# Kernel tuning notes

Hardware: AMD Instinct MI355X
Metric: run time of the kernel (lower is better)

Reference implementation:

```python
import jax, jax.numpy as jnp
import numpy as np

MODEL_DIM = 1024
BATCH, SEQ = 4, 2048


def setup_inputs() -> dict:
    key = jax.random.key(0)
    kx, kq, kk, kv = jax.random.split(key, 4)
    s = 1.0 / np.sqrt(MODEL_DIM)
    return {
        "x": jax.random.normal(kx, (BATCH, SEQ, MODEL_DIM), dtype=jnp.float32),
        "Wq": jax.random.normal(kq, (MODEL_DIM, MODEL_DIM), dtype=jnp.float32) * s,
        "Wk": jax.random.normal(kk, (MODEL_DIM, MODEL_DIM), dtype=jnp.float32) * s,
        "Wv": jax.random.normal(kv, (MODEL_DIM, MODEL_DIM), dtype=jnp.float32) * s,
    }


def reference(x, Wq, Wk, Wv):
    # nn.Linear(d, d, bias=False): y = x @ W.T ; W stored [out, in]
    q = jnp.einsum("bsd,ed->bse", x, Wq)
    k = jnp.einsum("bsd,ed->bse", x, Wk)
    v = jnp.einsum("bsd,ed->bse", x, Wv)
    scores = jnp.einsum("bqd,bkd->bqk", q, k) / jnp.sqrt(jnp.float32(MODEL_DIM))
    attn = jax.nn.softmax(scores, axis=-1)
    return jnp.einsum("bqk,bkd->bqd", attn, v)
```

## Files before the change

### kernel.cpp

```cpp
#include <hip/hip_runtime.h>
#include <hip/hip_bf16.h>


typedef short bf16x8_t __attribute__((ext_vector_type(8)));
typedef float f32x4_t __attribute__((ext_vector_type(4)));
typedef unsigned short u16x8_t __attribute__((ext_vector_type(8)));

static __device__ __forceinline__ unsigned short f2bf(float f) {
  __hip_bfloat16 h = __float2bfloat16(f);
  return *reinterpret_cast<unsigned short*>(&h);
}

#define GLOAD_LDS16(gp, lp)                                            \
  __builtin_amdgcn_global_load_lds(                                    \
      (const __attribute__((address_space(1))) void*)(gp),             \
      (__attribute__((address_space(3))) void*)(lp), 16, 0, 0)

__global__ __launch_bounds__(256) void cast_f32_bf16(
    const float* __restrict__ in, unsigned short* __restrict__ out, int n8) {
  int i = blockIdx.x * 256 + threadIdx.x;
  if (i >= n8) return;
  float4 a = ((const float4*)in)[i * 2];
  float4 b = ((const float4*)in)[i * 2 + 1];
  u16x8_t o;
  o[0] = f2bf(a.x); o[1] = f2bf(a.y); o[2] = f2bf(a.z); o[3] = f2bf(a.w);
  o[4] = f2bf(b.x); o[5] = f2bf(b.y); o[6] = f2bf(b.z); o[7] = f2bf(b.w);
  ((u16x8_t*)out)[i] = o;
}

__global__ __launch_bounds__(256) void cast_w3(
    const float* __restrict__ Wq, const float* __restrict__ Wk,
    const float* __restrict__ Wv, unsigned short* __restrict__ Wqk,
    unsigned short* __restrict__ Wvb) {
  int i = blockIdx.x * 256 + threadIdx.x;
  int seg = i >> 17;
  int local = i & 131071;
  const float* src = (seg == 0) ? Wq : ((seg == 1) ? Wk : Wv);
  unsigned short* dst =
      (seg == 0) ? Wqk : ((seg == 1) ? (Wqk + 1048576) : Wvb);
  float4 a = ((const float4*)src)[local * 2];
  float4 b = ((const float4*)src)[local * 2 + 1];
  u16x8_t o;
  o[0] = f2bf(a.x); o[1] = f2bf(a.y); o[2] = f2bf(a.z); o[3] = f2bf(a.w);
  o[4] = f2bf(b.x); o[5] = f2bf(b.y); o[6] = f2bf(b.z); o[7] = f2bf(b.w);
  ((u16x8_t*)dst)[local] = o;
}

__global__ __launch_bounds__(256) void zero_f32(float* __restrict__ p, int n) {
  int i = blockIdx.x * 256 + threadIdx.x;
  if (i < n) p[i] = 0.0f;
}

template <int EPI>
__global__ __launch_bounds__(512, 2) void gemm256_nt(
    const unsigned short* __restrict__ A, const unsigned short* __restrict__ B,
    unsigned short* __restrict__ C, float* __restrict__ rowsum, int K,
    int lda, int ldb, int ldc, long long sA, long long sB, long long sC,
    float alpha, int rsz) {
  __shared__ unsigned short lds[2][2][256 * 64];

  const int gx = gridDim.x, gy = gridDim.y;
  const int nwg = gx * gy * gridDim.z;
  const int orig = (blockIdx.z * gy + blockIdx.y) * gx + blockIdx.x;
  const int swz = (orig & 7) * (nwg >> 3) + (orig >> 3);
  const int bx = swz % gx;
  const int tmp = swz / gx;
  const int by = tmp % gy;
  const int z = tmp / gy;

  const int tid = threadIdx.x;
  const int lane = tid & 63;
  const int w = tid >> 6;
  const int wm = w >> 2, wn = w & 3;
  const int m0 = by * 256, n0 = bx * 256;

  A += (long long)z * sA;
  B += (long long)z * sB;

  int sar[4], sac[4];
#pragma unroll
  for (int i = 0; i < 4; ++i) {
    int p = i * 512 + w * 64 + lane;
    int r = p >> 3;
    sar[i] = r;
    sac[i] = ((p & 7) ^ (r & 7)) * 8;
  }

  const int q = lane >> 4, rl = lane & 15;
  int aoff[8][2], boff[4][2];
#pragma unroll
  for (int t = 0; t < 8; ++t)
#pragma unroll
    for (int ks = 0; ks < 2; ++ks) {
      int ra = wm * 128 + t * 16 + rl;
      int ca = ks * 4 + q;
      aoff[t][ks] = ra * 64 + ((ca ^ (ra & 7)) * 8);
    }
#pragma unroll
  for (int u = 0; u < 4; ++u)
#pragma unroll
    for (int ks = 0; ks < 2; ++ks) {
      int rb = wn * 64 + u * 16 + rl;
      int ca = ks * 4 + q;
      boff[u][ks] = rb * 64 + ((ca ^ (rb & 7)) * 8);
    }

  f32x4_t acc[8][4];
#pragma unroll
  for (int i = 0; i < 8; ++i)
#pragma unroll
    for (int j = 0; j < 4; ++j) acc[i][j] = (f32x4_t){0.f, 0.f, 0.f, 0.f};

#define STAGE256(bufi, k0)                                                   \
  {                                                                          \
    _Pragma("unroll") for (int i = 0; i < 4; ++i)                            \
        GLOAD_LDS16(&A[(long long)(m0 + sar[i]) * lda + (k0) + sac[i]],      \
                    &lds[bufi][0][(i * 512 + w * 64) * 8]);                  \
    _Pragma("unroll") for (int i = 0; i < 4; ++i)                            \
        GLOAD_LDS16(&B[(long long)(n0 + sar[i]) * ldb + (k0) + sac[i]],      \
                    &lds[bufi][1][(i * 512 + w * 64) * 8]);                  \
  }

  const int NT = K >> 6;
  STAGE256(0, 0);
  STAGE256(1, 64);

  for (int t = 0; t < NT; ++t) {
    const int cur = t & 1;
    if (t < NT - 1)
      asm volatile("s_waitcnt vmcnt(8)" ::: "memory");
    else
      asm volatile("s_waitcnt vmcnt(0)" ::: "memory");
    __builtin_amdgcn_s_barrier();
    __builtin_amdgcn_sched_barrier(0);
    const unsigned short* Al = &lds[cur][0][0];
    const unsigned short* Bl = &lds[cur][1][0];
#pragma unroll
    for (int ks = 0; ks < 2; ++ks) {
      bf16x8_t af[8], bg[4];
#pragma unroll
      for (int tt = 0; tt < 8; ++tt)
        af[tt] = *(const bf16x8_t*)&Al[aoff[tt][ks]];
#pragma unroll
      for (int u = 0; u < 4; ++u) bg[u] = *(const bf16x8_t*)&Bl[boff[u][ks]];
      __builtin_amdgcn_s_setprio(1);
#pragma unroll
      for (int i = 0; i < 8; ++i)
#pragma unroll
        for (int j = 0; j < 4; ++j)
          acc[i][j] = __builtin_amdgcn_mfma_f32_16x16x32_bf16(af[i], bg[j],
                                                              acc[i][j], 0, 0, 0);
      __builtin_amdgcn_s_setprio(0);
    }
    __builtin_amdgcn_sched_barrier(0);
    __builtin_amdgcn_s_barrier();
    __builtin_amdgcn_sched_barrier(0);
    if (t + 2 < NT) STAGE256(cur, (t + 2) * 64);
  }

  if (EPI == 0) {
#pragma unroll
    for (int tt = 0; tt < 8; ++tt)
#pragma unroll
      for (int u = 0; u < 4; ++u)
#pragma unroll
        for (int j = 0; j < 4; ++j) {
          int row = m0 + wm * 128 + tt * 16 + q * 4 + j;
          int col = n0 + wn * 64 + u * 16 + rl;
          C[(long long)z * sC + (long long)row * ldc + col] =
              f2bf(acc[tt][u][j] * alpha);
        }
  } else {
#pragma unroll
    for (int tt = 0; tt < 8; ++tt)
#pragma unroll
      for (int j = 0; j < 4; ++j) {
        int row = m0 + wm * 128 + tt * 16 + q * 4 + j;
        float sum = 0.f;
#pragma unroll
        for (int u = 0; u < 4; ++u) {
          float e = __expf(acc[tt][u][j] * alpha);
          int col = n0 + wn * 64 + u * 16 + rl;
          C[(long long)z * sC + (long long)row * ldc + col] = f2bf(e);
          sum += e;
        }
#pragma unroll
        for (int mk = 1; mk <= 8; mk <<= 1) sum += __shfl_xor(sum, mk);
        if (rl == 0) atomicAdd(&rowsum[z * rsz + row], sum);
      }
  }
#undef STAGE256
}

template <int EPI, int BN>
__global__ __launch_bounds__(256) void gemm_nt(
    const unsigned short* __restrict__ A, const unsigned short* __restrict__ B,
    void* __restrict__ Cv, const float* __restrict__ rowsum, int M, int N,
    int K, int lda, int ldb, int ldc, long long sA, long long sB,
    long long sC, float alpha, int rsz) {
  constexpr int NB = BN / 32;
  __shared__ unsigned short As[128 * 64];
  __shared__ unsigned short Bs[BN * 64];

  const int gx = gridDim.x, gy = gridDim.y;
  const int nwg = gx * gy * gridDim.z;
  const int orig = (blockIdx.z * gy + blockIdx.y) * gx + blockIdx.x;
  const int swz = (orig & 7) * (nwg >> 3) + (orig >> 3);
  const int bx = swz % gx;
  const int tmp = swz / gx;
  const int by = tmp % gy;
  const int z = tmp / gy;

  const int tid = threadIdx.x;
  const int lane = tid & 63;
  const int w = tid >> 6;
  const int wm = w >> 1, wn = w & 1;
  const int m0 = by * 128;
  const int n0 = bx * BN;

  A += (long long)z * sA;
  B += (long long)z * sB;

  int sarow[4], sacol[4];
#pragma unroll
  for (int i = 0; i < 4; ++i) {
    int p = w * 256 + i * 64 + lane;
    int r = p >> 3;
    sarow[i] = r;
    sacol[i] = ((p & 7) ^ (r & 7)) * 8;
  }
  int sbrow[NB], sbcol[NB];
#pragma unroll
  for (int i = 0; i < NB; ++i) {
    int p = w * (BN * 2) + i * 64 + lane;
    int r = p >> 3;
    sbrow[i] = r;
    sbcol[i] = ((p & 7) ^ (r & 7)) * 8;
  }

  const int q = lane >> 4, rl = lane & 15;
  int aoff[4][2], boff[NB][2];
#pragma unroll
  for (int t = 0; t < 4; ++t)
#pragma unroll
    for (int ks = 0; ks < 2; ++ks) {
      int ra = wm * 64 + t * 16 + rl;
      int ca = ks * 4 + q;
      aoff[t][ks] = ra * 64 + ((ca ^ (ra & 7)) * 8);
    }
#pragma unroll
  for (int u = 0; u < NB; ++u)
#pragma unroll
    for (int ks = 0; ks < 2; ++ks) {
      int rb = wn * (BN / 2) + u * 16 + rl;
      int ca = ks * 4 + q;
      boff[u][ks] = rb * 64 + ((ca ^ (rb & 7)) * 8);
    }

  f32x4_t acc[4][NB];
#pragma unroll
  for (int i = 0; i < 4; ++i)
#pragma unroll
    for (int j = 0; j < NB; ++j) acc[i][j] = (f32x4_t){0.f, 0.f, 0.f, 0.f};

  for (int k0 = 0; k0 < K; k0 += 64) {
    __syncthreads();
#pragma unroll
    for (int i = 0; i < 4; ++i) {
      GLOAD_LDS16(&A[(long long)(m0 + sarow[i]) * lda + k0 + sacol[i]],
                  &As[(w * 4 + i) * 512]);
    }
#pragma unroll
    for (int i = 0; i < NB; ++i) {
      GLOAD_LDS16(&B[(long long)(n0 + sbrow[i]) * ldb + k0 + sbcol[i]],
                  &Bs[(w * NB + i) * 512]);
    }
    __syncthreads();

#pragma unroll
    for (int ks = 0; ks < 2; ++ks) {
      bf16x8_t af[4], bg[NB];
#pragma unroll
      for (int t = 0; t < 4; ++t) af[t] = *(const bf16x8_t*)&As[aoff[t][ks]];
#pragma unroll
      for (int u = 0; u < NB; ++u) bg[u] = *(const bf16x8_t*)&Bs[boff[u][ks]];
#pragma unroll
      for (int i = 0; i < 4; ++i)
#pragma unroll
        for (int j = 0; j < NB; ++j)
          acc[i][j] = __builtin_amdgcn_mfma_f32_16x16x32_bf16(af[i], bg[j],
                                                              acc[i][j], 0, 0, 0);
    }
  }

#pragma unroll
  for (int t = 0; t < 4; ++t)
#pragma unroll
    for (int u = 0; u < NB; ++u)
#pragma unroll
      for (int j = 0; j < 4; ++j) {
        int row = m0 + wm * 64 + t * 16 + q * 4 + j;
        int col = n0 + wn * (BN / 2) + u * 16 + rl;
        if (EPI == 0) {
          ((unsigned short*)Cv)[(long long)z * sC + (long long)row * ldc +
                                col] = f2bf(acc[t][u][j] * alpha);
        } else if (EPI == 1) {
          ((float*)Cv)[(long long)z * sC + (long long)row * ldc + col] =
              acc[t][u][j] * alpha;
        } else {
          float inv = 1.0f / rowsum[z * rsz + row];
          ((float*)Cv)[(long long)z * sC + (long long)row * ldc + col] =
              acc[t][u][j] * inv;
        }
      }
}

extern "C" void kernel_launch(void* const* d_in, const int* in_sizes, int n_in,
                              void* d_out, int out_size, void* d_ws,
                              size_t ws_size, hipStream_t stream) {
  const float* x = (const float*)d_in[0];
  const float* Wq = (const float*)d_in[1];
  const float* Wk = (const float*)d_in[2];
  const float* Wv = (const float*)d_in[3];
  float* out = (float*)d_out;

  unsigned short* xb = (unsigned short*)d_ws;
  unsigned short* Wqk = xb + 8388608;
  unsigned short* Wvb = Wqk + 2097152;
  unsigned short* Cqk = Wvb + 1048576;
  unsigned short* VTb = Cqk + 16777216;
  unsigned short* Scb = VTb + 8388608;
  float* rowsumf = (float*)(Scb + 16777216);

  const dim3 blk(256);
  const dim3 blk512(512);

  cast_f32_bf16<<<4096, blk, 0, stream>>>(x, xb, 1048576);
  cast_w3<<<1536, blk, 0, stream>>>(Wq, Wk, Wv, Wqk, Wvb);
  zero_f32<<<32, blk, 0, stream>>>(rowsumf, 8192);

  gemm256_nt<0><<<dim3(8, 32, 1), blk512, 0, stream>>>(
      xb, Wqk, Cqk, nullptr, 1024, 1024, 1024, 2048, 0, 0, 0, 1.0f, 0);

  gemm_nt<0, 128><<<dim3(64, 8, 1), blk, 0, stream>>>(
      Wvb, xb, VTb, nullptr, 1024, 8192, 1024, 1024, 1024, 8192, 0, 0, 0,
      1.0f, 0);

  gemm256_nt<1><<<dim3(8, 8, 4), blk512, 0, stream>>>(
      Cqk, Cqk + 1024, Scb, rowsumf, 1024, 2048, 2048, 2048,
      (long long)2048 * 2048, (long long)2048 * 2048, (long long)2048 * 2048,
      0.03125f, 2048);

  gemm_nt<2, 64><<<dim3(16, 16, 4), blk, 0, stream>>>(
      Scb, VTb, out, rowsumf, 2048, 1024, 2048, 2048, 8192, 1024,
      (long long)2048 * 2048, 2048, (long long)2048 * 1024, 1.0f, 2048);
}
```

Baseline: 169.7 us.

## Split 256-tile GEMM into four-phase pipelined quadrants and use it for PV

The 256-row GEMM main loop is restructured into four MFMA phases over quadrants of the tile, each with its own barrier. Global-to-LDS loads for the next k-steps are issued in halves between phases so memory traffic interleaves with matrix math. The kernel is templated on N tile width and gains a normalizing fp32 epilogue, so the final attention-times-V GEMM now runs on 256x128 tiles with 512 threads instead of the small 128x64 kernel. The extra barriers and finer-grained vmcnt waits add synchronization, and the load ordering is tricky to get right.

```diff
diff --git a/kernel.cpp b/kernel.cpp
--- a/kernel.cpp
+++ b/kernel.cpp
@@ -51,13 +51,20 @@
   if (i < n) p[i] = 0.0f;
 }
 
-template <int EPI>
-__global__ __launch_bounds__(512, 2) void gemm256_nt(
+template <int EPI, int BN>
+__global__ __launch_bounds__(512, 2) void gemm256p(
     const unsigned short* __restrict__ A, const unsigned short* __restrict__ B,
-    unsigned short* __restrict__ C, float* __restrict__ rowsum, int K,
-    int lda, int ldb, int ldc, long long sA, long long sB, long long sC,
-    float alpha, int rsz) {
-  __shared__ unsigned short lds[2][2][256 * 64];
+    void* __restrict__ Cv, float* __restrict__ rowsum, int K, int lda,
+    int ldb, int ldc, long long sA, long long sB, long long sC, float alpha,
+    int rsz) {
+  constexpr int NBG = BN / 64;
+  constexpr int NH = NBG / 2;
+  constexpr int BL = BN / 128;
+  constexpr int BNW = BN / 4;
+  constexpr int ASZ = 256 * 64;
+  constexpr int BSZ = BN * 64;
+
+  __shared__ unsigned short lds[2][ASZ + BSZ];
 
   const int gx = gridDim.x, gy = gridDim.y;
   const int nwg = gx * gy * gridDim.z;
@@ -72,105 +79,160 @@
   const int lane = tid & 63;
   const int w = tid >> 6;
   const int wm = w >> 2, wn = w & 3;
-  const int m0 = by * 256, n0 = bx * 256;
+  const int m0 = by * 256, n0 = bx * BN;
 
   A += (long long)z * sA;
   B += (long long)z * sB;
 
-  int sar[4], sac[4];
-#pragma unroll
-  for (int i = 0; i < 4; ++i) {
-    int p = i * 512 + w * 64 + lane;
-    int r = p >> 3;
-    sar[i] = r;
-    sac[i] = ((p & 7) ^ (r & 7)) * 8;
-  }
+  int sta_row[2][2], sta_col[2][2], sta_lds[2][2];
+#pragma unroll
+  for (int mh = 0; mh < 2; ++mh)
+#pragma unroll
+    for (int i = 0; i < 2; ++i) {
+      int j = w * 2 + i;
+      int l0 = (j >> 3) * 1024 + mh * 512 + (j & 7) * 64;
+      int lf = l0 + lane;
+      int R = lf >> 3;
+      sta_row[mh][i] = R;
+      sta_col[mh][i] = ((lf & 7) ^ (R & 7)) * 8;
+      sta_lds[mh][i] = l0 * 8;
+    }
+  int stb_row[2][BL], stb_col[2][BL], stb_lds[2][BL];
+#pragma unroll
+  for (int nh = 0; nh < 2; ++nh)
+#pragma unroll
+    for (int i = 0; i < BL; ++i) {
+      int l0;
+      if (BL == 2) {
+        int j = w * 2 + i;
+        l0 = (j >> 2) * 512 + nh * 256 + (j & 3) * 64;
+      } else {
+        int j = w;
+        l0 = (j >> 1) * 256 + nh * 128 + (j & 1) * 64;
+      }
+      int lf = l0 + lane;
+      int R = lf >> 3;
+      stb_row[nh][i] = R;
+      stb_col[nh][i] = ((lf & 7) ^ (R & 7)) * 8;
+      stb_lds[nh][i] = ASZ + l0 * 8;
+    }
 
   const int q = lane >> 4, rl = lane & 15;
-  int aoff[8][2], boff[4][2];
-#pragma unroll
-  for (int t = 0; t < 8; ++t)
+  int aoff[8][2], boff[NBG][2];
+#pragma unroll
+  for (int tt = 0; tt < 8; ++tt)
 #pragma unroll
     for (int ks = 0; ks < 2; ++ks) {
-      int ra = wm * 128 + t * 16 + rl;
-      int ca = ks * 4 + q;
-      aoff[t][ks] = ra * 64 + ((ca ^ (ra & 7)) * 8);
-    }
-#pragma unroll
-  for (int u = 0; u < 4; ++u)
+      int ra = wm * 128 + tt * 16 + rl;
+      aoff[tt][ks] = ra * 64 + (((ks * 4 + q) ^ (ra & 7)) * 8);
+    }
+#pragma unroll
+  for (int u = 0; u < NBG; ++u)
 #pragma unroll
     for (int ks = 0; ks < 2; ++ks) {
-      int rb = wn * 64 + u * 16 + rl;
-      int ca = ks * 4 + q;
-      boff[u][ks] = rb * 64 + ((ca ^ (rb & 7)) * 8);
-    }
-
-  f32x4_t acc[8][4];
+      int rb = wn * BNW + u * 16 + rl;
+      boff[u][ks] = ASZ + rb * 64 + (((ks * 4 + q) ^ (rb & 7)) * 8);
+    }
+
+  f32x4_t acc[8][NBG];
 #pragma unroll
   for (int i = 0; i < 8; ++i)
 #pragma unroll
-    for (int j = 0; j < 4; ++j) acc[i][j] = (f32x4_t){0.f, 0.f, 0.f, 0.f};
-
-#define STAGE256(bufi, k0)                                                   \
-  {                                                                          \
-    _Pragma("unroll") for (int i = 0; i < 4; ++i)                            \
-        GLOAD_LDS16(&A[(long long)(m0 + sar[i]) * lda + (k0) + sac[i]],      \
-                    &lds[bufi][0][(i * 512 + w * 64) * 8]);                  \
-    _Pragma("unroll") for (int i = 0; i < 4; ++i)                            \
-        GLOAD_LDS16(&B[(long long)(n0 + sar[i]) * ldb + (k0) + sac[i]],      \
-                    &lds[bufi][1][(i * 512 + w * 64) * 8]);                  \
-  }
+    for (int j = 0; j < NBG; ++j) acc[i][j] = (f32x4_t){0.f, 0.f, 0.f, 0.f};
+
+#define SA(BUFI, MH, K0)                                                    \
+  {                                                                         \
+    _Pragma("unroll") for (int i_ = 0; i_ < 2; ++i_)                        \
+        GLOAD_LDS16(&A[(long long)(m0 + sta_row[MH][i_]) * lda + (K0) +     \
+                       sta_col[MH][i_]],                                    \
+                    &lds[BUFI][sta_lds[MH][i_]]);                           \
+  }
+#define SB(BUFI, NH_, K0)                                                   \
+  {                                                                         \
+    _Pragma("unroll") for (int i_ = 0; i_ < BL; ++i_)                       \
+        GLOAD_LDS16(&B[(long long)(n0 + stb_row[NH_][i_]) * ldb + (K0) +    \
+                       stb_col[NH_][i_]],                                   \
+                    &lds[BUFI][stb_lds[NH_][i_]]);                          \
+  }
+#define LDAF(MH)                                                            \
+  _Pragma("unroll") for (int i_ = 0; i_ < 4; ++i_)                          \
+  _Pragma("unroll") for (int ks_ = 0; ks_ < 2; ++ks_)                       \
+      af[i_][ks_] = *(const bf16x8_t*)&L[aoff[(MH)*4 + i_][ks_]];
+#define LDBG(NH_)                                                           \
+  _Pragma("unroll") for (int j_ = 0; j_ < NH; ++j_)                         \
+  _Pragma("unroll") for (int ks_ = 0; ks_ < 2; ++ks_)                       \
+      bg[j_][ks_] = *(const bf16x8_t*)&L[boff[(NH_)*NH + j_][ks_]];
+#define PH_MFMA(MH, NH_)                                                    \
+  __builtin_amdgcn_s_barrier();                                             \
+  asm volatile("s_waitcnt lgkmcnt(0)" ::: "memory");                        \
+  __builtin_amdgcn_sched_barrier(0);                                        \
+  __builtin_amdgcn_s_setprio(1);                                            \
+  _Pragma("unroll") for (int ks_ = 0; ks_ < 2; ++ks_)                       \
+  _Pragma("unroll") for (int i_ = 0; i_ < 4; ++i_)                          \
+  _Pragma("unroll") for (int j_ = 0; j_ < NH; ++j_)                         \
+      acc[(MH)*4 + i_][(NH_)*NH + j_] =                                     \
+          __builtin_amdgcn_mfma_f32_16x16x32_bf16(                          \
+              af[i_][ks_], bg[j_][ks_], acc[(MH)*4 + i_][(NH_)*NH + j_],    \
+              0, 0, 0);                                                     \
+  __builtin_amdgcn_s_setprio(0);                                            \
+  __builtin_amdgcn_sched_barrier(0);                                        \
+  __builtin_amdgcn_s_barrier();                                             \
+  __builtin_amdgcn_sched_barrier(0);
 
   const int NT = K >> 6;
-  STAGE256(0, 0);
-  STAGE256(1, 64);
+
+  SA(0, 0, 0); SA(0, 1, 0); SB(0, 0, 0); SB(0, 1, 0);
+  SA(1, 0, 64); SB(1, 1, 64);
+  if (BL == 2)
+    asm volatile("s_waitcnt vmcnt(4)" ::: "memory");
+  else
+    asm volatile("s_waitcnt vmcnt(3)" ::: "memory");
+  __builtin_amdgcn_s_barrier();
+  __builtin_amdgcn_sched_barrier(0);
+
+  bf16x8_t af[4][2], bg[NH][2];
 
   for (int t = 0; t < NT; ++t) {
-    const int cur = t & 1;
-    if (t < NT - 1)
-      asm volatile("s_waitcnt vmcnt(8)" ::: "memory");
-    else
+    const int bu = t & 1, nx = bu ^ 1;
+    const unsigned short* L = lds[bu];
+    const bool p1 = (t + 1 < NT), p2 = (t + 2 < NT);
+    LDAF(0);
+    LDBG(0);
+    if (p1) SA(nx, 1, (t + 1) * 64);
+    PH_MFMA(0, 0);
+    LDBG(1);
+    if (p1) SB(nx, 0, (t + 1) * 64);
+    PH_MFMA(0, 1);
+    LDAF(1);
+    if (p2) SA(bu, 0, (t + 2) * 64);
+    PH_MFMA(1, 1);
+    LDBG(0);
+    if (p2) {
+      SB(bu, 1, (t + 2) * 64);
+      if (BL == 2)
+        asm volatile("s_waitcnt vmcnt(4)" ::: "memory");
+      else
+        asm volatile("s_waitcnt vmcnt(3)" ::: "memory");
+    } else {
       asm volatile("s_waitcnt vmcnt(0)" ::: "memory");
-    __builtin_amdgcn_s_barrier();
-    __builtin_amdgcn_sched_barrier(0);
-    const unsigned short* Al = &lds[cur][0][0];
-    const unsigned short* Bl = &lds[cur][1][0];
-#pragma unroll
-    for (int ks = 0; ks < 2; ++ks) {
-      bf16x8_t af[8], bg[4];
-#pragma unroll
-      for (int tt = 0; tt < 8; ++tt)
-        af[tt] = *(const bf16x8_t*)&Al[aoff[tt][ks]];
-#pragma unroll
-      for (int u = 0; u < 4; ++u) bg[u] = *(const bf16x8_t*)&Bl[boff[u][ks]];
-      __builtin_amdgcn_s_setprio(1);
-#pragma unroll
-      for (int i = 0; i < 8; ++i)
-#pragma unroll
-        for (int j = 0; j < 4; ++j)
-          acc[i][j] = __builtin_amdgcn_mfma_f32_16x16x32_bf16(af[i], bg[j],
-                                                              acc[i][j], 0, 0, 0);
-      __builtin_amdgcn_s_setprio(0);
-    }
-    __builtin_amdgcn_sched_barrier(0);
-    __builtin_amdgcn_s_barrier();
-    __builtin_amdgcn_sched_barrier(0);
-    if (t + 2 < NT) STAGE256(cur, (t + 2) * 64);
+    }
+    PH_MFMA(1, 0);
   }
 
   if (EPI == 0) {
+    unsigned short* C = (unsigned short*)Cv + (long long)z * sC;
 #pragma unroll
     for (int tt = 0; tt < 8; ++tt)
 #pragma unroll
-      for (int u = 0; u < 4; ++u)
+      for (int u = 0; u < NBG; ++u)
 #pragma unroll
         for (int j = 0; j < 4; ++j) {
           int row = m0 + wm * 128 + tt * 16 + q * 4 + j;
-          int col = n0 + wn * 64 + u * 16 + rl;
-          C[(long long)z * sC + (long long)row * ldc + col] =
-              f2bf(acc[tt][u][j] * alpha);
+          int col = n0 + wn * BNW + u * 16 + rl;
+          C[(long long)row * ldc + col] = f2bf(acc[tt][u][j] * alpha);
         }
-  } else {
+  } else if (EPI == 1) {
+    unsigned short* C = (unsigned short*)Cv + (long long)z * sC;
 #pragma unroll
     for (int tt = 0; tt < 8; ++tt)
 #pragma unroll
@@ -178,68 +240,69 @@
         int row = m0 + wm * 128 + tt * 16 + q * 4 + j;
         float sum = 0.f;
 #pragma unroll
-        for (int u = 0; u < 4; ++u) {
+        for (int u = 0; u < NBG; ++u) {
           float e = __expf(acc[tt][u][j] * alpha);
-          int col = n0 + wn * 64 + u * 16 + rl;
-          C[(long long)z * sC + (long long)row * ldc + col] = f2bf(e);
+          int col = n0 + wn * BNW + u * 16 + rl;
+          C[(long long)row * ldc + col] = f2bf(e);
           sum += e;
         }
 #pragma unroll
         for (int mk = 1; mk <= 8; mk <<= 1) sum += __shfl_xor(sum, mk);
         if (rl == 0) atomicAdd(&rowsum[z * rsz + row], sum);
       }
-  }
-#undef STAGE256
-}
-
-template <int EPI, int BN>
-__global__ __launch_bounds__(256) void gemm_nt(
+  } else {
+    float* C = (float*)Cv + (long long)z * sC;
+#pragma unroll
+    for (int tt = 0; tt < 8; ++tt)
+#pragma unroll
+      for (int j = 0; j < 4; ++j) {
+        int row = m0 + wm * 128 + tt * 16 + q * 4 + j;
+        float inv = 1.0f / rowsum[z * rsz + row];
+#pragma unroll
+        for (int u = 0; u < NBG; ++u) {
+          int col = n0 + wn * BNW + u * 16 + rl;
+          C[(long long)row * ldc + col] = acc[tt][u][j] * inv;
+        }
+      }
+  }
+#undef SA
+#undef SB
+#undef LDAF
+#undef LDBG
+#undef PH_MFMA
+}
+
+__global__ __launch_bounds__(256) void gemm_nt128(
     const unsigned short* __restrict__ A, const unsigned short* __restrict__ B,
-    void* __restrict__ Cv, const float* __restrict__ rowsum, int M, int N,
-    int K, int lda, int ldb, int ldc, long long sA, long long sB,
-    long long sC, float alpha, int rsz) {
-  constexpr int NB = BN / 32;
+    unsigned short* __restrict__ C, int K, int lda, int ldb, int ldc) {
   __shared__ unsigned short As[128 * 64];
-  __shared__ unsigned short Bs[BN * 64];
+  __shared__ unsigned short Bs[128 * 64];
 
   const int gx = gridDim.x, gy = gridDim.y;
-  const int nwg = gx * gy * gridDim.z;
-  const int orig = (blockIdx.z * gy + blockIdx.y) * gx + blockIdx.x;
+  const int nwg = gx * gy;
+  const int orig = blockIdx.y * gx + blockIdx.x;
   const int swz = (orig & 7) * (nwg >> 3) + (orig >> 3);
   const int bx = swz % gx;
-  const int tmp = swz / gx;
-  const int by = tmp % gy;
-  const int z = tmp / gy;
+  const int by = swz / gx;
 
   const int tid = threadIdx.x;
   const int lane = tid & 63;
   const int w = tid >> 6;
   const int wm = w >> 1, wn = w & 1;
   const int m0 = by * 128;
-  const int n0 = bx * BN;
-
-  A += (long long)z * sA;
-  B += (long long)z * sB;
-
-  int sarow[4], sacol[4];
+  const int n0 = bx * 128;
+
+  int srow[4], scol[4];
 #pragma unroll
   for (int i = 0; i < 4; ++i) {
     int p = w * 256 + i * 64 + lane;
     int r = p >> 3;
-    sarow[i] = r;
-    sacol[i] = ((p & 7) ^ (r & 7)) * 8;
-  }
-  int sbrow[NB], sbcol[NB];
-#pragma unroll
-  for (int i = 0; i < NB; ++i) {
-    int p = w * (BN * 2) + i * 64 + lane;
-    int r = p >> 3;
-    sbrow[i] = r;
-    sbcol[i] = ((p & 7) ^ (r & 7)) * 8;
+    srow[i] = r;
+    scol[i] = ((p & 7) ^ (r & 7)) * 8;
   }
 
   const int q = lane >> 4, rl = lane & 15;
-  int aoff[4][2], boff[NB][2];
+  int aoff[4][2], boff[4][2];
 #pragma unroll
   for (int t = 0; t < 4; ++t)
 #pragma unroll
@@ -247,71 +310,52 @@
       int ra = wm * 64 + t * 16 + rl;
       int ca = ks * 4 + q;
       aoff[t][ks] = ra * 64 + ((ca ^ (ra & 7)) * 8);
-    }
-#pragma unroll
-  for (int u = 0; u < NB; ++u)
-#pragma unroll
-    for (int ks = 0; ks < 2; ++ks) {
-      int rb = wn * (BN / 2) + u * 16 + rl;
-      int ca = ks * 4 + q;
-      boff[u][ks] = rb * 64 + ((ca ^ (rb & 7)) * 8);
-    }
-
-  f32x4_t acc[4][NB];
+      int rb = wn * 64 + t * 16 + rl;
+      boff[t][ks] = rb * 64 + ((ca ^ (rb & 7)) * 8);
+    }
+
+  f32x4_t acc[4][4];
 #pragma unroll
   for (int i = 0; i < 4; ++i)
 #pragma unroll
-    for (int j = 0; j < NB; ++j) acc[i][j] = (f32x4_t){0.f, 0.f, 0.f, 0.f};
+    for (int j = 0; j < 4; ++j) acc[i][j] = (f32x4_t){0.f, 0.f, 0.f, 0.f};
 
   for (int k0 = 0; k0 < K; k0 += 64) {
     __syncthreads();
 #pragma unroll
     for (int i = 0; i < 4; ++i) {
-      GLOAD_LDS16(&A[(long long)(m0 + sarow[i]) * lda + k0 + sacol[i]],
+      GLOAD_LDS16(&A[(long long)(m0 + srow[i]) * lda + k0 + scol[i]],
                   &As[(w * 4 + i) * 512]);
-    }
-#pragma unroll
-    for (int i = 0; i < NB; ++i) {
-      GLOAD_LDS16(&B[(long long)(n0 + sbrow[i]) * ldb + k0 + sbcol[i]],
-                  &Bs[(w * NB + i) * 512]);
+      GLOAD_LDS16(&B[(long long)(n0 + srow[i]) * ldb + k0 + scol[i]],
+                  &Bs[(w * 4 + i) * 512]);
     }
     __syncthreads();
 
 #pragma unroll
     for (int ks = 0; ks < 2; ++ks) {
-      bf16x8_t af[4], bg[NB];
+      bf16x8_t af[4], bgv[4];
 #pragma unroll
       for (int t = 0; t < 4; ++t) af[t] = *(const bf16x8_t*)&As[aoff[t][ks]];
 #pragma unroll
-      for (int u = 0; u < NB; ++u) bg[u] = *(const bf16x8_t*)&Bs[boff[u][ks]];
+      for (int u = 0; u < 4; ++u) bgv[u] = *(const bf16x8_t*)&Bs[boff[u][ks]];
 #pragma unroll
       for (int i = 0; i < 4; ++i)
 #pragma unroll
-        for (int j = 0; j < NB; ++j)
-          acc[i][j] = __builtin_amdgcn_mfma_f32_16x16x32_bf16(af[i], bg[j],
-                                                              acc[i][j], 0, 0, 0);
+        for (int j = 0; j < 4; ++j)
+          acc[i][j] = __builtin_amdgcn_mfma_f32_16x16x32_bf16(
+              af[i], bgv[j], acc[i][j], 0, 0, 0);
     }
   }
 
 #pragma unroll
   for (int t = 0; t < 4; ++t)
 #pragma unroll
-    for (int u = 0; u < NB; ++u)
+    for (int u = 0; u < 4; ++u)
 #pragma unroll
       for (int j = 0; j < 4; ++j) {
         int row = m0 + wm * 64 + t * 16 + q * 4 + j;
-        int col = n0 + wn * (BN / 2) + u * 16 + rl;
-        if (EPI == 0) {
-          ((unsigned short*)Cv)[(long long)z * sC + (long long)row * ldc +
-                                col] = f2bf(acc[t][u][j] * alpha);
-        } else if (EPI == 1) {
-          ((float*)Cv)[(long long)z * sC + (long long)row * ldc + col] =
-              acc[t][u][j] * alpha;
-        } else {
-          float inv = 1.0f / rowsum[z * rsz + row];
-          ((float*)Cv)[(long long)z * sC + (long long)row * ldc + col] =
-              acc[t][u][j] * inv;
-        }
+        int col = n0 + wn * 64 + u * 16 + rl;
+        C[(long long)row * ldc + col] = f2bf(acc[t][u][j]);
       }
 }
 
@@ -339,19 +383,18 @@
   cast_w3<<<1536, blk, 0, stream>>>(Wq, Wk, Wv, Wqk, Wvb);
   zero_f32<<<32, blk, 0, stream>>>(rowsumf, 8192);
 
-  gemm256_nt<0><<<dim3(8, 32, 1), blk512, 0, stream>>>(
+  gemm256p<0, 256><<<dim3(8, 32, 1), blk512, 0, stream>>>(
       xb, Wqk, Cqk, nullptr, 1024, 1024, 1024, 2048, 0, 0, 0, 1.0f, 0);
 
-  gemm_nt<0, 128><<<dim3(64, 8, 1), blk, 0, stream>>>(
-      Wvb, xb, VTb, nullptr, 1024, 8192, 1024, 1024, 1024, 8192, 0, 0, 0,
-      1.0f, 0);
-
-  gemm256_nt<1><<<dim3(8, 8, 4), blk512, 0, stream>>>(
+  gemm_nt128<<<dim3(64, 8), blk, 0, stream>>>(Wvb, xb, VTb, 1024, 1024, 1024,
+                                              8192);
+
+  gemm256p<1, 256><<<dim3(8, 8, 4), blk512, 0, stream>>>(
       Cqk, Cqk + 1024, Scb, rowsumf, 1024, 2048, 2048, 2048,
       (long long)2048 * 2048, (long long)2048 * 2048, (long long)2048 * 2048,
       0.03125f, 2048);
 
-  gemm_nt<2, 64><<<dim3(16, 16, 4), blk, 0, stream>>>(
-      Scb, VTb, out, rowsumf, 2048, 1024, 2048, 2048, 8192, 1024,
+  gemm256p<2, 128><<<dim3(8, 8, 4), blk512, 0, stream>>>(
+      Scb, VTb, out, rowsumf, 2048, 2048, 8192, 1024,
       (long long)2048 * 2048, 2048, (long long)2048 * 1024, 1.0f, 2048);
 }
```

Result: faster. 164.0 us (-3.3%).
